# Kernel optimization log

Measured on AMD Instinct MI355X. Metric: run time of the kernel, lower is better.

The kernel has to match this reference:

```python
import jax, jax.numpy as jnp
import numpy as np

B, T, I, H, O = 64, 512, 512, 1024, 512


def _lstm_layer(x_seq, W_ih, W_hh, b_ih, b_hh):
    # x_seq: [B, T, D_in]; PyTorch LSTMCell gate order: i, f, g, o
    bsz = x_seq.shape[0]
    hid = W_hh.shape[1]
    # Precompute input projection for all timesteps as one big GEMM
    x_proj = jnp.einsum('btd,gd->btg', x_seq, W_ih) + b_ih + b_hh  # [B, T, 4H]

    def step(carry, xp_t):
        h, c = carry
        gates = xp_t + h @ W_hh.T  # [B, 4H]
        i_g, f_g, g_g, o_g = jnp.split(gates, 4, axis=-1)
        i_g = jax.nn.sigmoid(i_g)
        f_g = jax.nn.sigmoid(f_g)
        g_g = jnp.tanh(g_g)
        o_g = jax.nn.sigmoid(o_g)
        c_new = f_g * c + i_g * g_g
        h_new = o_g * jnp.tanh(c_new)
        return (h_new, c_new), h_new

    h0 = jnp.zeros((bsz, hid), dtype=x_seq.dtype)
    c0 = jnp.zeros((bsz, hid), dtype=x_seq.dtype)
    (_, _), hs = jax.lax.scan(step, (h0, c0), jnp.swapaxes(x_proj, 0, 1))
    return jnp.swapaxes(hs, 0, 1)  # [B, T, H]


def setup_inputs() -> dict:
    key = jax.random.key(0)
    ks = jax.random.split(key, 12)
    s1 = 1.0 / np.sqrt(H)
    x = jax.random.normal(ks[0], (B, T, I), dtype=jnp.float32)
    W_ih1 = jax.random.uniform(ks[1], (4 * H, I), jnp.float32, -s1, s1)
    W_hh1 = jax.random.uniform(ks[2], (4 * H, H), jnp.float32, -s1, s1)
    b_ih1 = jax.random.uniform(ks[3], (4 * H,), jnp.float32, -s1, s1)
    b_hh1 = jax.random.uniform(ks[4], (4 * H,), jnp.float32, -s1, s1)
    W_ih2 = jax.random.uniform(ks[5], (4 * H, H), jnp.float32, -s1, s1)
    W_hh2 = jax.random.uniform(ks[6], (4 * H, H), jnp.float32, -s1, s1)
    b_ih2 = jax.random.uniform(ks[7], (4 * H,), jnp.float32, -s1, s1)
    b_hh2 = jax.random.uniform(ks[8], (4 * H,), jnp.float32, -s1, s1)
    fc_W = jax.random.uniform(ks[9], (O, H), jnp.float32, -s1, s1)
    fc_b = jax.random.uniform(ks[10], (O,), jnp.float32, -s1, s1)
    return {"x": x, "W_ih1": W_ih1, "W_hh1": W_hh1, "b_ih1": b_ih1, "b_hh1": b_hh1,
            "W_ih2": W_ih2, "W_hh2": W_hh2, "b_ih2": b_ih2, "b_hh2": b_hh2,
            "fc_W": fc_W, "fc_b": fc_b}


def reference(x, W_ih1, W_hh1, b_ih1, b_hh1, W_ih2, W_hh2, b_ih2, b_hh2, fc_W, fc_b):
    h1s = _lstm_layer(x, W_ih1, W_hh1, b_ih1, b_hh1)   # [B, T, H]
    h2s = _lstm_layer(h1s, W_ih2, W_hh2, b_ih2, b_hh2)  # [B, T, H]
    out = jnp.einsum('bth,oh->bto', h2s, fc_W) + fc_b   # [B, T, O]
    return out
```

## Files before the change

kernel.cpp:

```cpp
#include <hip/hip_runtime.h>
#include <hip/hip_bf16.h>
#include <math.h>

#define B_  64
#define T_  512
#define I_  512
#define H_  1024
#define G4_ 4096
#define O_  512
#define TC_ 64
#define NCH (T_ / TC_)
#define WPG 16

typedef short  s16x8 __attribute__((ext_vector_type(8)));
typedef float  fx4   __attribute__((ext_vector_type(4)));
typedef float  fx8   __attribute__((ext_vector_type(8)));
typedef unsigned short u16;
typedef u16    u16x4 __attribute__((ext_vector_type(4)));
typedef unsigned long long u64t;

__device__ __forceinline__ u16 f2bf(float f){
  unsigned u = __float_as_uint(f);
  unsigned r = u + 0x7fffu + ((u >> 16) & 1u);
  return (u16)(r >> 16);
}
__device__ __forceinline__ float bf2f(u16 s){ return __uint_as_float(((unsigned)s) << 16); }
__device__ __forceinline__ float sigm(float x){ return 1.0f / (1.0f + __expf(-x)); }
__device__ __forceinline__ float tanh_(float x){
  float ax = fabsf(x);
  float e  = __expf(2.0f * ax);
  float r  = 1.0f - 2.0f / (e + 1.0f);
  return copysignf(r, x);
}
__device__ __forceinline__ fx4 mfma(s16x8 a, s16x8 b, fx4 c){
  return __builtin_amdgcn_mfma_f32_16x16x32_bf16(a, b, c, 0, 0, 0);
}
__device__ __forceinline__ void keepreg(s16x8& v){ asm volatile("" : "+v"(v)); }

__device__ __forceinline__ void lds_cp16(const u16* g, short* l){
  __builtin_amdgcn_global_load_lds(
      (const __attribute__((address_space(1))) void*)g,
      (__attribute__((address_space(3))) void*)l, 16, 0, 0);
}

__device__ __forceinline__ u64t aload64(const u16* p){
  return __hip_atomic_load((const u64t*)p, __ATOMIC_RELAXED, __HIP_MEMORY_SCOPE_SYSTEM);
}
__device__ __forceinline__ void astore32(u16* p, unsigned v){
  __hip_atomic_store((unsigned*)p, v, __ATOMIC_RELAXED, __HIP_MEMORY_SCOPE_SYSTEM);
}
__device__ __forceinline__ unsigned aload32(const unsigned* p){
  return __hip_atomic_load(p, __ATOMIC_RELAXED, __HIP_MEMORY_SCOPE_SYSTEM);
}
__device__ __forceinline__ unsigned afadd(unsigned* p){
  return __hip_atomic_fetch_add(p, 1u, __ATOMIC_RELAXED, __HIP_MEMORY_SCOPE_SYSTEM);
}

__global__ void cvt_hilo(const float* __restrict__ src, u16* __restrict__ hi,
                         u16* __restrict__ lo, int n4){
  int i      = blockIdx.x * blockDim.x + threadIdx.x;
  int stride = gridDim.x * blockDim.x;
  for (; i < n4; i += stride){
    fx4 v = ((const fx4*)src)[i];
    u16x4 h, l;
    #pragma unroll
    for (int k = 0; k < 4; ++k){
      u16 hh = f2bf(v[k]);
      h[k] = hh;
      l[k] = f2bf(v[k] - bf2f(hh));
    }
    ((u16x4*)hi)[i] = h;
    ((u16x4*)lo)[i] = l;
  }
}

__global__ void vadd(const float* __restrict__ a, const float* __restrict__ b,
                     float* __restrict__ o, int n){
  int i = blockIdx.x * blockDim.x + threadIdx.x;
  if (i < n) o[i] = a[i] + b[i];
}

template<int KD, int AMODE, int OMODE>
__global__ __launch_bounds__(256)
void gemm128(const float* __restrict__ Af,
             const u16* __restrict__ Ah, const u16* __restrict__ Al,
             const u16* __restrict__ Bh, const u16* __restrict__ Bl,
             const float* __restrict__ bias,
             float* __restrict__ out, int N, int c0)
{
  __shared__ short As0[4096], As1[4096];
  __shared__ short Bs0[4096], Bs1[4096];
  __shared__ float xt[(OMODE == 0) ? 64 * 130 : 4];

  const int tid  = threadIdx.x;
  const int w    = tid >> 6;
  const int lane = tid & 63;
  const int l15  = lane & 15;
  const int lhi  = lane >> 4;
  const int mb   = blockIdx.x * 128;
  const int nb   = blockIdx.y * 128;

  const int srow  = lane >> 2;
  const int skc   = lane & 3;
  const int sslot = srow * 32 + skc * 8;

  fx4 acc[4][4] = {};

  for (int kt = 0; kt < KD / 32; ++kt){
    const int kk = kt * 32 + skc * 8;
    __syncthreads();
    #pragma unroll
    for (int bi = 0; bi < 2; ++bi){
      const int bl   = 2 * w + bi;
      const int lrow = bl * 16 + srow;
      const int r    = mb + lrow;
      const int b    = r & 63;
      const int tlr  = r >> 6;
      const size_t bo = (size_t)(nb + bl * 16 + srow) * KD + kk;
      lds_cp16(Bh + bo, &Bs0[bl * 512]);
      lds_cp16(Bl + bo, &Bs1[bl * 512]);
      if (AMODE == 0){
        const float* p = Af + ((size_t)b * T_ + c0 + tlr) * KD + kk;
        fx8 v = *reinterpret_cast<const fx8*>(p);
        s16x8 hv, lv;
        #pragma unroll
        for (int q = 0; q < 8; ++q){
          u16 hh = f2bf(v[q]);
          hv[q] = (short)hh;
          lv[q] = (short)f2bf(v[q] - bf2f(hh));
        }
        *reinterpret_cast<s16x8*>(&As0[bl * 512 + sslot]) = hv;
        *reinterpret_cast<s16x8*>(&As1[bl * 512 + sslot]) = lv;
      } else {
        const size_t ao = ((size_t)b * TC_ + tlr) * KD + kk;
        lds_cp16(Ah + ao, &As0[bl * 512]);
        lds_cp16(Al + ao, &As1[bl * 512]);
      }
    }
    __syncthreads();

    const int fro = l15 * 32 + lhi * 8;
    s16x8 bhf[4], blf[4];
    #pragma unroll
    for (int j = 0; j < 4; ++j){
      const int bb = ((w >> 1) * 4 + j) * 512 + fro;
      bhf[j] = *reinterpret_cast<const s16x8*>(&Bs0[bb]);
      blf[j] = *reinterpret_cast<const s16x8*>(&Bs1[bb]);
    }
    #pragma unroll
    for (int i = 0; i < 4; ++i){
      const int ab = ((w & 1) * 4 + i) * 512 + fro;
      s16x8 ah = *reinterpret_cast<const s16x8*>(&As0[ab]);
      s16x8 al = *reinterpret_cast<const s16x8*>(&As1[ab]);
      #pragma unroll
      for (int j = 0; j < 4; ++j){
        acc[i][j] = mfma(ah, bhf[j], acc[i][j]);
        acc[i][j] = mfma(ah, blf[j], acc[i][j]);
        acc[i][j] = mfma(al, bhf[j], acc[i][j]);
      }
    }
  }

  if (OMODE == 0){
    #pragma unroll
    for (int p = 0; p < 2; ++p){
      __syncthreads();
      if ((w & 1) == p){
        #pragma unroll
        for (int i = 0; i < 4; ++i)
          #pragma unroll
          for (int j = 0; j < 4; ++j){
            const int col = (w >> 1) * 64 + j * 16 + l15;
            const float bv = bias[nb + col];
            #pragma unroll
            for (int r = 0; r < 4; ++r)
              xt[(i * 16 + lhi * 4 + r) * 130 + col] = acc[i][j][r] + bv;
          }
      }
      __syncthreads();
      const int tlv = (mb >> 6) + p;
      const int b   = tid & 63;
      #pragma unroll
      for (int c = 0; c < 32; ++c){
        const int col = (tid >> 6) + c * 4;
        const int n = nb + col;
        const int g = n >> 10;
        const int jj = n & 1023;
        out[((size_t)(tlv * 4 + g) * H_ + jj) * 64 + b] = xt[b * 130 + col];
      }
    }
  } else {
    #pragma unroll
    for (int j = 0; j < 4; ++j){
      const int n = nb + (w >> 1) * 64 + j * 16 + l15;
      const float bv = bias[n];
      #pragma unroll
      for (int i = 0; i < 4; ++i)
        #pragma unroll
        for (int r = 0; r < 4; ++r){
          const int m  = mb + (w & 1) * 64 + i * 16 + lhi * 4 + r;
          const int b  = m & 63;
          const int tlv = m >> 6;
          out[((size_t)b * T_ + c0 + tlv) * (size_t)N + n] = acc[i][j][r] + bv;
        }
    }
  }
}

__device__ __forceinline__ void gbar(unsigned* bar, int gid, unsigned ep, int ngrp){
  if (afadd(&bar[gid * 32]) == WPG - 1u){
    __hip_atomic_store(&bar[gid * 32], 0u, __ATOMIC_RELAXED, __HIP_MEMORY_SCOPE_SYSTEM);
    if (afadd(&bar[512]) == (unsigned)(ngrp - 1)){
      __hip_atomic_store(&bar[512], 0u, __ATOMIC_RELAXED, __HIP_MEMORY_SCOPE_SYSTEM);
      astore32((u16*)&bar[544], ep);
    } else {
      while (aload32(&bar[544]) != ep) __builtin_amdgcn_s_sleep(1);
    }
    astore32((u16*)&bar[1024 + gid * 32], ep);
  } else {
    while (aload32(&bar[1024 + gid * 32]) != ep) __builtin_amdgcn_s_sleep(1);
  }
}

#define RSTR 577
__global__ __launch_bounds__(512) __attribute__((amdgpu_waves_per_eu(2, 2)))
void lstm_pd(int mode, unsigned ep0, int ngrp,
    const u16* __restrict__ W1h, const u16* __restrict__ W1l,
    const float* __restrict__ xp1, float* __restrict__ cst1,
    u16* __restrict__ hx1h, u16* __restrict__ hx1l,
    u16* __restrict__ ha1h, u16* __restrict__ ha1l,
    const u16* __restrict__ W2h, const u16* __restrict__ W2l,
    const float* __restrict__ xp2, float* __restrict__ cst2,
    u16* __restrict__ hx2h, u16* __restrict__ hx2l,
    u16* __restrict__ ha2h, u16* __restrict__ ha2l,
    unsigned* __restrict__ bar)
{
  __shared__ float red[16 * RSTR];

  const int x8 = blockIdx.x & 7;
  const int q  = blockIdx.x >> 3;
  int part, m4, ghi;
  if (mode == 3){ part = q & 1;    m4 = (q >> 1) & 3; ghi = q >> 3; }
  else          { part = mode - 1; m4 = q & 3;        ghi = q >> 2; }
  const int jb  = (x8 + 8 * ghi) * 32;
  const int mb  = m4 * 16;
  const int gid = blockIdx.x >> 4;

  const u16*   Wh  = part ? W2h  : W1h;
  const u16*   Wl  = part ? W2l  : W1l;
  const float* xp  = part ? xp2  : xp1;
  float*       cst = part ? cst2 : cst1;
  u16*         hxh = part ? hx2h : hx1h;
  u16*         hxl = part ? hx2l : hx1l;
  u16*         hah = part ? ha2h : ha1h;
  u16*         hal = part ? ha2l : ha1l;

  const int tid  = threadIdx.x;
  const int lane = tid & 63;
  const int wv   = tid >> 6;
  const int l15  = lane & 15;
  const int lhi  = lane >> 4;
  const int kb0  = wv * 128 + lhi * 8;

  size_t wrowR[4], wrowS[4];
  #pragma unroll
  for (int ct = 0; ct < 4; ++ct){
    const int clR = ct * 16 + l15;
    const int clS = (ct + 4) * 16 + l15;
    wrowR[ct] = (size_t)((clR >> 5) * H_ + jb + (clR & 31));
    wrowS[ct] = (size_t)((clS >> 5) * H_ + jb + (clS & 31));
  }

  s16x8 wrh[4][4], wrl[4][4];
  #pragma unroll
  for (int ct = 0; ct < 4; ++ct)
    #pragma unroll
    for (int s = 0; s < 4; ++s){
      const size_t wo = wrowR[ct] * H_ + kb0 + s * 32;
      wrh[ct][s] = *reinterpret_cast<const s16x8*>(Wh + wo);
      wrl[ct][s] = *reinterpret_cast<const s16x8*>(Wl + wo);
      keepreg(wrh[ct][s]);
      keepreg(wrl[ct][s]);
    }

  const int up = tid & 15;
  const int mm = tid >> 4;
  const int u0 = 2 * up;
  const int j0 = jb + u0;
  const int eb = mb + mm;
  float cva = 0.0f, cvb = 0.0f;
  if (tid < 256){
    cva = cst[(size_t)j0 * B_ + eb];
    cvb = cst[(size_t)(j0 + 1) * B_ + eb];
  }

  for (int tl = 0; tl < TC_; ++tl){
    const int par = tl & 1;
    const u16* rph = hxh + par * (64 * H_);
    const u16* rpl = hxl + par * (64 * H_);
    u16* nph = hxh + (par ^ 1) * (64 * H_);
    u16* npl = hxl + (par ^ 1) * (64 * H_);

    float xq0[4], xq1[4];
    if (tid < 256){
      #pragma unroll
      for (int g = 0; g < 4; ++g){
        const float* xr = xp + ((size_t)(tl * 4 + g) * H_ + j0) * 64 + eb;
        xq0[g] = xr[0];
        xq1[g] = xr[64];
      }
    }

    fx4 acc[8] = {};
    #pragma unroll
    for (int s = 0; s < 4; ++s){
      const int kb = kb0 + s * 32;
      const u16* ph = rph + (size_t)(mb + l15) * H_ + kb;
      const u16* pl = rpl + (size_t)(mb + l15) * H_ + kb;
      union { u64t u[2]; s16x8 v; } ua, ul;
      ua.u[0] = aload64(ph);  ua.u[1] = aload64(ph + 4);
      ul.u[0] = aload64(pl);  ul.u[1] = aload64(pl + 4);
      #pragma unroll
      for (int ct = 0; ct < 4; ++ct){
        acc[ct] = mfma(ua.v, wrh[ct][s], acc[ct]);
        acc[ct] = mfma(ua.v, wrl[ct][s], acc[ct]);
        acc[ct] = mfma(ul.v, wrh[ct][s], acc[ct]);
      }
      #pragma unroll
      for (int ct = 0; ct < 4; ++ct){
        const size_t wo = wrowS[ct] * H_ + kb;
        s16x8 bh = *reinterpret_cast<const s16x8*>(Wh + wo);
        s16x8 bl = *reinterpret_cast<const s16x8*>(Wl + wo);
        acc[4 + ct] = mfma(ua.v, bh, acc[4 + ct]);
        acc[4 + ct] = mfma(ua.v, bl, acc[4 + ct]);
        acc[4 + ct] = mfma(ul.v, bh, acc[4 + ct]);
      }
    }

    #pragma unroll
    for (int ct = 0; ct < 4; ++ct)
      #pragma unroll
      for (int r = 0; r < 4; ++r)
        red[(lhi * 4 + r) * RSTR + (ct * 16 + l15) * 9 + wv] = acc[ct][r];
    __syncthreads();
    float i0s = 0, i1s = 0, f0s = 0, f1s = 0;
    if (tid < 256){
      const float* r0 = red + mm * RSTR + (u0) * 9;
      const float* r1 = red + mm * RSTR + (u0 + 1) * 9;
      const float* r2 = red + mm * RSTR + (32 + u0) * 9;
      const float* r3 = red + mm * RSTR + (32 + u0 + 1) * 9;
      #pragma unroll
      for (int w = 0; w < 8; ++w){
        i0s += r0[w]; i1s += r1[w]; f0s += r2[w]; f1s += r3[w];
      }
    }
    __syncthreads();

    #pragma unroll
    for (int ct = 0; ct < 4; ++ct)
      #pragma unroll
      for (int r = 0; r < 4; ++r)
        red[(lhi * 4 + r) * RSTR + (ct * 16 + l15) * 9 + wv] = acc[4 + ct][r];
    __syncthreads();

    if (tid < 256){
      float g0s = 0, g1s = 0, o0s = 0, o1s = 0;
      const float* r0 = red + mm * RSTR + (u0) * 9;
      const float* r1 = red + mm * RSTR + (u0 + 1) * 9;
      const float* r2 = red + mm * RSTR + (32 + u0) * 9;
      const float* r3 = red + mm * RSTR + (32 + u0 + 1) * 9;
      #pragma unroll
      for (int w = 0; w < 8; ++w){
        g0s += r0[w]; g1s += r1[w]; o0s += r2[w]; o1s += r3[w];
      }
      float iv = sigm (i0s + xq0[0]);
      float fv = sigm (f0s + xq0[1]);
      float gv = tanh_(g0s + xq0[2]);
      float ov = sigm (o0s + xq0[3]);
      float cn = fv * cva + iv * gv;
      float h0 = ov * tanh_(cn);
      cva = cn;
      iv = sigm (i1s + xq1[0]);
      fv = sigm (f1s + xq1[1]);
      gv = tanh_(g1s + xq1[2]);
      ov = sigm (o1s + xq1[3]);
      cn = fv * cvb + iv * gv;
      float h1 = ov * tanh_(cn);
      cvb = cn;

      u16 h0h = f2bf(h0), h0l = f2bf(h0 - bf2f(h0h));
      u16 h1h = f2bf(h1), h1l = f2bf(h1 - bf2f(h1h));
      astore32(nph + (size_t)eb * H_ + j0, (unsigned)h0h | ((unsigned)h1h << 16));
      astore32(npl + (size_t)eb * H_ + j0, (unsigned)h0l | ((unsigned)h1l << 16));
      const size_t ai = ((size_t)eb * TC_ + tl) * H_ + j0;
      *(unsigned*)(hah + ai) = (unsigned)h0h | ((unsigned)h1h << 16);
      *(unsigned*)(hal + ai) = (unsigned)h0l | ((unsigned)h1l << 16);
    }

    __syncthreads();
    if (tid == 0) gbar(bar, gid, ep0 + tl + 1, ngrp);
    __syncthreads();
  }
  if (tid < 256){
    cst[(size_t)j0 * B_ + eb]       = cva;
    cst[(size_t)(j0 + 1) * B_ + eb] = cvb;
  }
}

extern "C" void kernel_launch(void* const* d_in, const int* in_sizes, int n_in,
                              void* d_out, int out_size, void* d_ws, size_t ws_size,
                              hipStream_t stream)
{
  const float* x    = (const float*)d_in[0];
  const float* Wih1 = (const float*)d_in[1];
  const float* Whh1 = (const float*)d_in[2];
  const float* bih1 = (const float*)d_in[3];
  const float* bhh1 = (const float*)d_in[4];
  const float* Wih2 = (const float*)d_in[5];
  const float* Whh2 = (const float*)d_in[6];
  const float* bih2 = (const float*)d_in[7];
  const float* bhh2 = (const float*)d_in[8];
  const float* fcW  = (const float*)d_in[9];
  const float* fcb  = (const float*)d_in[10];
  float* out = (float*)d_out;
  (void)in_sizes; (void)n_in; (void)out_size; (void)ws_size;

  char* base = (char*)d_ws;
  size_t off = 0;
  auto alloc = [&](size_t bytes) -> void* {
    void* p = base + off;
    off = (off + bytes + 255) & ~(size_t)255;
    return p;
  };
  u16* Wih1_hi = (u16*)alloc((size_t)G4_ * I_ * 2);
  u16* Wih1_lo = (u16*)alloc((size_t)G4_ * I_ * 2);
  u16* Whh1_hi = (u16*)alloc((size_t)G4_ * H_ * 2);
  u16* Whh1_lo = (u16*)alloc((size_t)G4_ * H_ * 2);
  u16* Wih2_hi = (u16*)alloc((size_t)G4_ * H_ * 2);
  u16* Wih2_lo = (u16*)alloc((size_t)G4_ * H_ * 2);
  u16* Whh2_hi = (u16*)alloc((size_t)G4_ * H_ * 2);
  u16* Whh2_lo = (u16*)alloc((size_t)G4_ * H_ * 2);
  u16* fcW_hi  = (u16*)alloc((size_t)O_ * H_ * 2);
  u16* fcW_lo  = (u16*)alloc((size_t)O_ * H_ * 2);
  float* bsum1 = (float*)alloc((size_t)G4_ * 4);
  float* bsum2 = (float*)alloc((size_t)G4_ * 4);
  float* cst1  = (float*)alloc((size_t)B_ * H_ * 4);
  float* cst2  = (float*)alloc((size_t)B_ * H_ * 4);
  u16* hx1h = (u16*)alloc((size_t)2 * B_ * H_ * 2);
  u16* hx1l = (u16*)alloc((size_t)2 * B_ * H_ * 2);
  u16* hx2h = (u16*)alloc((size_t)2 * B_ * H_ * 2);
  u16* hx2l = (u16*)alloc((size_t)2 * B_ * H_ * 2);
  u16* h1s_hi = (u16*)alloc((size_t)B_ * TC_ * H_ * 2);
  u16* h1s_lo = (u16*)alloc((size_t)B_ * TC_ * H_ * 2);
  u16* h2s_hi = (u16*)alloc((size_t)B_ * TC_ * H_ * 2);
  u16* h2s_lo = (u16*)alloc((size_t)B_ * TC_ * H_ * 2);
  float* xp1  = (float*)alloc((size_t)TC_ * G4_ * B_ * 4);
  float* xp2  = (float*)alloc((size_t)TC_ * G4_ * B_ * 4);
  unsigned* bar = (unsigned*)alloc(2048 * 4);

  cvt_hilo<<<512, 256, 0, stream>>>(Wih1, Wih1_hi, Wih1_lo, G4_ * I_ / 4);
  cvt_hilo<<<512, 256, 0, stream>>>(Whh1, Whh1_hi, Whh1_lo, G4_ * H_ / 4);
  cvt_hilo<<<512, 256, 0, stream>>>(Wih2, Wih2_hi, Wih2_lo, G4_ * H_ / 4);
  cvt_hilo<<<512, 256, 0, stream>>>(Whh2, Whh2_hi, Whh2_lo, G4_ * H_ / 4);
  cvt_hilo<<<256, 256, 0, stream>>>(fcW,  fcW_hi,  fcW_lo,  O_ * H_ / 4);
  vadd<<<16, 256, 0, stream>>>(bih1, bhh1, bsum1, G4_);
  vadd<<<16, 256, 0, stream>>>(bih2, bhh2, bsum2, G4_);

  hipMemsetAsync(cst1, 0, (size_t)B_ * H_ * 4, stream);
  hipMemsetAsync(cst2, 0, (size_t)B_ * H_ * 4, stream);
  hipMemsetAsync(hx1h, 0, (size_t)2 * B_ * H_ * 2, stream);
  hipMemsetAsync(hx1l, 0, (size_t)2 * B_ * H_ * 2, stream);
  hipMemsetAsync(hx2h, 0, (size_t)2 * B_ * H_ * 2, stream);
  hipMemsetAsync(hx2l, 0, (size_t)2 * B_ * H_ * 2, stream);
  hipMemsetAsync(bar,  0, 2048 * 4, stream);

  const dim3 gX(32, 32);
  const dim3 gF(32, 4);

  gemm128<I_, 0, 0><<<gX, 256, 0, stream>>>(
      x, nullptr, nullptr, Wih1_hi, Wih1_lo, bsum1, xp1, G4_, 0);

  unsigned ep = 0;
  for (int c = 0; c <= NCH; ++c){
    const int mode = ((c < NCH) ? 1 : 0) | ((c >= 1) ? 2 : 0);
    const int nwg  = (mode == 3) ? 256 : 128;
    int ngrp = nwg / WPG;
    {
      void* args[] = { (void*)&mode, (void*)&ep, (void*)&ngrp,
                       (void*)&Whh1_hi, (void*)&Whh1_lo, (void*)&xp1, (void*)&cst1,
                       (void*)&hx1h, (void*)&hx1l, (void*)&h1s_hi, (void*)&h1s_lo,
                       (void*)&Whh2_hi, (void*)&Whh2_lo, (void*)&xp2, (void*)&cst2,
                       (void*)&hx2h, (void*)&hx2l, (void*)&h2s_hi, (void*)&h2s_lo,
                       (void*)&bar };
      hipLaunchCooperativeKernel((const void*)lstm_pd, dim3(nwg), dim3(512),
                                 args, 0, stream);
      ep += TC_;
    }
    if (c < NCH)
      gemm128<H_, 1, 0><<<gX, 256, 0, stream>>>(
          nullptr, h1s_hi, h1s_lo, Wih2_hi, Wih2_lo, bsum2, xp2, G4_, 0);
    if (c + 1 < NCH)
      gemm128<I_, 0, 0><<<gX, 256, 0, stream>>>(
          x, nullptr, nullptr, Wih1_hi, Wih1_lo, bsum1, xp1, G4_, (c + 1) * TC_);
    if (c >= 1)
      gemm128<H_, 1, 1><<<gF, 256, 0, stream>>>(
          nullptr, h2s_hi, h2s_lo, fcW_hi, fcW_lo, fcb, out, O_, (c - 1) * TC_);
  }
}
```

Measured before the change: 10.14 ms.

## Run both LSTM layers in 1024-thread blocks with per-half layer split

The recurrent kernel now always launches 256 workgroups of 1024 threads. Each half of a workgroup handles one LSTM layer, and a mode bit can idle a half. Each block covers 16 hidden units instead of 32, and the weights are streamed from global memory every step instead of being pinned in registers. This is meant to spread the recurrent work across more CUs and cut register pressure. In exchange it reloads weights every timestep, issues narrower 16-bit atomic stores and leaves half-idle blocks in the first and last chunks.

Result: slower. 20.78 ms (+105.0%).

```diff
diff --git a/kernel.cpp b/kernel.cpp
--- a/kernel.cpp
+++ b/kernel.cpp
@@ -35,7 +35,6 @@
 __device__ __forceinline__ fx4 mfma(s16x8 a, s16x8 b, fx4 c){
   return __builtin_amdgcn_mfma_f32_16x16x32_bf16(a, b, c, 0, 0, 0);
 }
-__device__ __forceinline__ void keepreg(s16x8& v){ asm volatile("" : "+v"(v)); }
 
 __device__ __forceinline__ void lds_cp16(const u16* g, short* l){
   __builtin_amdgcn_global_load_lds(
@@ -48,6 +47,9 @@
 }
 __device__ __forceinline__ void astore32(u16* p, unsigned v){
   __hip_atomic_store((unsigned*)p, v, __ATOMIC_RELAXED, __HIP_MEMORY_SCOPE_SYSTEM);
+}
+__device__ __forceinline__ void astore16(u16* p, u16 v){
+  __hip_atomic_store(p, v, __ATOMIC_RELAXED, __HIP_MEMORY_SCOPE_SYSTEM);
 }
 __device__ __forceinline__ unsigned aload32(const unsigned* p){
   return __hip_atomic_load(p, __ATOMIC_RELAXED, __HIP_MEMORY_SCOPE_SYSTEM);
@@ -210,21 +212,21 @@
 __device__ __forceinline__ void gbar(unsigned* bar, int gid, unsigned ep, int ngrp){
   if (afadd(&bar[gid * 32]) == WPG - 1u){
     __hip_atomic_store(&bar[gid * 32], 0u, __ATOMIC_RELAXED, __HIP_MEMORY_SCOPE_SYSTEM);
-    if (afadd(&bar[512]) == (unsigned)(ngrp - 1)){
-      __hip_atomic_store(&bar[512], 0u, __ATOMIC_RELAXED, __HIP_MEMORY_SCOPE_SYSTEM);
-      astore32((u16*)&bar[544], ep);
+    if (afadd(&bar[1024]) == (unsigned)(ngrp - 1)){
+      __hip_atomic_store(&bar[1024], 0u, __ATOMIC_RELAXED, __HIP_MEMORY_SCOPE_SYSTEM);
+      astore32((u16*)&bar[1056], ep);
     } else {
-      while (aload32(&bar[544]) != ep) __builtin_amdgcn_s_sleep(1);
-    }
-    astore32((u16*)&bar[1024 + gid * 32], ep);
+      while (aload32(&bar[1056]) != ep) __builtin_amdgcn_s_sleep(1);
+    }
+    astore32((u16*)&bar[2048 + gid * 32], ep);
   } else {
-    while (aload32(&bar[1024 + gid * 32]) != ep) __builtin_amdgcn_s_sleep(1);
+    while (aload32(&bar[2048 + gid * 32]) != ep) __builtin_amdgcn_s_sleep(1);
   }
 }
 
 #define RSTR 577
-__global__ __launch_bounds__(512) __attribute__((amdgpu_waves_per_eu(2, 2)))
-void lstm_pd(int mode, unsigned ep0, int ngrp,
+__global__ __launch_bounds__(1024)
+void lstm_pd3(int mode, unsigned ep0, int ngrp,
     const u16* __restrict__ W1h, const u16* __restrict__ W1l,
     const float* __restrict__ xp1, float* __restrict__ cst1,
     u16* __restrict__ hx1h, u16* __restrict__ hx1l,
@@ -235,64 +237,46 @@
     u16* __restrict__ ha2h, u16* __restrict__ ha2l,
     unsigned* __restrict__ bar)
 {
-  __shared__ float red[16 * RSTR];
-
-  const int x8 = blockIdx.x & 7;
-  const int q  = blockIdx.x >> 3;
-  int part, m4, ghi;
-  if (mode == 3){ part = q & 1;    m4 = (q >> 1) & 3; ghi = q >> 3; }
-  else          { part = mode - 1; m4 = q & 3;        ghi = q >> 2; }
-  const int jb  = (x8 + 8 * ghi) * 32;
-  const int mb  = m4 * 16;
-  const int gid = blockIdx.x >> 4;
-
-  const u16*   Wh  = part ? W2h  : W1h;
-  const u16*   Wl  = part ? W2l  : W1l;
-  const float* xp  = part ? xp2  : xp1;
-  float*       cst = part ? cst2 : cst1;
-  u16*         hxh = part ? hx2h : hx1h;
-  u16*         hxl = part ? hx2l : hx1l;
-  u16*         hah = part ? ha2h : ha1h;
-  u16*         hal = part ? ha2l : ha1l;
+  __shared__ float red[2][16 * RSTR];
 
   const int tid  = threadIdx.x;
-  const int lane = tid & 63;
-  const int wv   = tid >> 6;
+  const int half = tid >> 9;
+  const int htid = tid & 511;
+  const int act  = (mode >> half) & 1;
+  const int gid  = blockIdx.x >> 4;
+  const int bx   = blockIdx.x;
+  const int m4   = bx & 3;
+  const int ug   = bx >> 2;
+  const int jb   = ug * 16;
+  const int mb   = m4 * 16;
+
+  const u16*   Wh  = half ? W2h  : W1h;
+  const u16*   Wl  = half ? W2l  : W1l;
+  const float* xp  = half ? xp2  : xp1;
+  float*       cst = half ? cst2 : cst1;
+  u16*         hxh = half ? hx2h : hx1h;
+  u16*         hxl = half ? hx2l : hx1l;
+  u16*         hah = half ? ha2h : ha1h;
+  u16*         hal = half ? ha2l : ha1l;
+  float*       rd  = red[half];
+
+  const int lane = htid & 63;
+  const int wv   = htid >> 6;
   const int l15  = lane & 15;
   const int lhi  = lane >> 4;
   const int kb0  = wv * 128 + lhi * 8;
 
-  size_t wrowR[4], wrowS[4];
-  #pragma unroll
-  for (int ct = 0; ct < 4; ++ct){
-    const int clR = ct * 16 + l15;
-    const int clS = (ct + 4) * 16 + l15;
-    wrowR[ct] = (size_t)((clR >> 5) * H_ + jb + (clR & 31));
-    wrowS[ct] = (size_t)((clS >> 5) * H_ + jb + (clS & 31));
-  }
-
-  s16x8 wrh[4][4], wrl[4][4];
+  size_t wrow[4];
   #pragma unroll
   for (int ct = 0; ct < 4; ++ct)
-    #pragma unroll
-    for (int s = 0; s < 4; ++s){
-      const size_t wo = wrowR[ct] * H_ + kb0 + s * 32;
-      wrh[ct][s] = *reinterpret_cast<const s16x8*>(Wh + wo);
-      wrl[ct][s] = *reinterpret_cast<const s16x8*>(Wl + wo);
-      keepreg(wrh[ct][s]);
-      keepreg(wrl[ct][s]);
-    }
-
-  const int up = tid & 15;
-  const int mm = tid >> 4;
-  const int u0 = 2 * up;
-  const int j0 = jb + u0;
+    wrow[ct] = (size_t)(ct * H_ + jb + l15);
+
+  const int uu = htid & 15;
+  const int mm = (htid >> 4) & 15;
+  const int j0 = jb + uu;
   const int eb = mb + mm;
-  float cva = 0.0f, cvb = 0.0f;
-  if (tid < 256){
-    cva = cst[(size_t)j0 * B_ + eb];
-    cvb = cst[(size_t)(j0 + 1) * B_ + eb];
-  }
+  float cva = 0.0f;
+  if (act && htid < 256) cva = cst[(size_t)j0 * B_ + eb];
 
   for (int tl = 0; tl < TC_; ++tl){
     const int par = tl & 1;
@@ -301,110 +285,72 @@
     u16* nph = hxh + (par ^ 1) * (64 * H_);
     u16* npl = hxl + (par ^ 1) * (64 * H_);
 
-    float xq0[4], xq1[4];
-    if (tid < 256){
+    float xq[4];
+    if (act && htid < 256){
+      #pragma unroll
+      for (int g = 0; g < 4; ++g)
+        xq[g] = xp[((size_t)(tl * 4 + g) * H_ + j0) * 64 + eb];
+    }
+
+    if (act){
+      fx4 acc[4] = {};
+      #pragma unroll
+      for (int s = 0; s < 4; ++s){
+        const int kb = kb0 + s * 32;
+        const u16* ph = rph + (size_t)(mb + l15) * H_ + kb;
+        const u16* pl = rpl + (size_t)(mb + l15) * H_ + kb;
+        union { u64t u[2]; s16x8 v; } ua, ul;
+        ua.u[0] = aload64(ph);  ua.u[1] = aload64(ph + 4);
+        ul.u[0] = aload64(pl);  ul.u[1] = aload64(pl + 4);
+        #pragma unroll
+        for (int ct = 0; ct < 4; ++ct){
+          const size_t wo = wrow[ct] * H_ + kb;
+          s16x8 bh = *reinterpret_cast<const s16x8*>(Wh + wo);
+          s16x8 bl = *reinterpret_cast<const s16x8*>(Wl + wo);
+          acc[ct] = mfma(ua.v, bh, acc[ct]);
+          acc[ct] = mfma(ua.v, bl, acc[ct]);
+          acc[ct] = mfma(ul.v, bh, acc[ct]);
+        }
+      }
+      #pragma unroll
+      for (int ct = 0; ct < 4; ++ct)
+        #pragma unroll
+        for (int r = 0; r < 4; ++r)
+          rd[(lhi * 4 + r) * RSTR + (ct * 16 + l15) * 9 + wv] = acc[ct][r];
+    }
+    __syncthreads();
+
+    if (act && htid < 256){
+      float gsum[4];
       #pragma unroll
       for (int g = 0; g < 4; ++g){
-        const float* xr = xp + ((size_t)(tl * 4 + g) * H_ + j0) * 64 + eb;
-        xq0[g] = xr[0];
-        xq1[g] = xr[64];
-      }
-    }
-
-    fx4 acc[8] = {};
-    #pragma unroll
-    for (int s = 0; s < 4; ++s){
-      const int kb = kb0 + s * 32;
-      const u16* ph = rph + (size_t)(mb + l15) * H_ + kb;
-      const u16* pl = rpl + (size_t)(mb + l15) * H_ + kb;
-      union { u64t u[2]; s16x8 v; } ua, ul;
-      ua.u[0] = aload64(ph);  ua.u[1] = aload64(ph + 4);
-      ul.u[0] = aload64(pl);  ul.u[1] = aload64(pl + 4);
-      #pragma unroll
-      for (int ct = 0; ct < 4; ++ct){
-        acc[ct] = mfma(ua.v, wrh[ct][s], acc[ct]);
-        acc[ct] = mfma(ua.v, wrl[ct][s], acc[ct]);
-        acc[ct] = mfma(ul.v, wrh[ct][s], acc[ct]);
-      }
-      #pragma unroll
-      for (int ct = 0; ct < 4; ++ct){
-        const size_t wo = wrowS[ct] * H_ + kb;
-        s16x8 bh = *reinterpret_cast<const s16x8*>(Wh + wo);
-        s16x8 bl = *reinterpret_cast<const s16x8*>(Wl + wo);
-        acc[4 + ct] = mfma(ua.v, bh, acc[4 + ct]);
-        acc[4 + ct] = mfma(ua.v, bl, acc[4 + ct]);
-        acc[4 + ct] = mfma(ul.v, bh, acc[4 + ct]);
-      }
-    }
-
-    #pragma unroll
-    for (int ct = 0; ct < 4; ++ct)
-      #pragma unroll
-      for (int r = 0; r < 4; ++r)
-        red[(lhi * 4 + r) * RSTR + (ct * 16 + l15) * 9 + wv] = acc[ct][r];
-    __syncthreads();
-    float i0s = 0, i1s = 0, f0s = 0, f1s = 0;
-    if (tid < 256){
-      const float* r0 = red + mm * RSTR + (u0) * 9;
-      const float* r1 = red + mm * RSTR + (u0 + 1) * 9;
-      const float* r2 = red + mm * RSTR + (32 + u0) * 9;
-      const float* r3 = red + mm * RSTR + (32 + u0 + 1) * 9;
-      #pragma unroll
-      for (int w = 0; w < 8; ++w){
-        i0s += r0[w]; i1s += r1[w]; f0s += r2[w]; f1s += r3[w];
-      }
-    }
-    __syncthreads();
-
-    #pragma unroll
-    for (int ct = 0; ct < 4; ++ct)
-      #pragma unroll
-      for (int r = 0; r < 4; ++r)
-        red[(lhi * 4 + r) * RSTR + (ct * 16 + l15) * 9 + wv] = acc[4 + ct][r];
-    __syncthreads();
-
-    if (tid < 256){
-      float g0s = 0, g1s = 0, o0s = 0, o1s = 0;
-      const float* r0 = red + mm * RSTR + (u0) * 9;
-      const float* r1 = red + mm * RSTR + (u0 + 1) * 9;
-      const float* r2 = red + mm * RSTR + (32 + u0) * 9;
-      const float* r3 = red + mm * RSTR + (32 + u0 + 1) * 9;
-      #pragma unroll
-      for (int w = 0; w < 8; ++w){
-        g0s += r0[w]; g1s += r1[w]; o0s += r2[w]; o1s += r3[w];
-      }
-      float iv = sigm (i0s + xq0[0]);
-      float fv = sigm (f0s + xq0[1]);
-      float gv = tanh_(g0s + xq0[2]);
-      float ov = sigm (o0s + xq0[3]);
+        const float* rp = rd + mm * RSTR + (g * 16 + uu) * 9;
+        float s = 0.0f;
+        #pragma unroll
+        for (int w = 0; w < 8; ++w) s += rp[w];
+        gsum[g] = s;
+      }
+      float iv = sigm (gsum[0] + xq[0]);
+      float fv = sigm (gsum[1] + xq[1]);
+      float gv = tanh_(gsum[2] + xq[2]);
+      float ov = sigm (gsum[3] + xq[3]);
       float cn = fv * cva + iv * gv;
-      float h0 = ov * tanh_(cn);
+      float hv = ov * tanh_(cn);
       cva = cn;
-      iv = sigm (i1s + xq1[0]);
-      fv = sigm (f1s + xq1[1]);
-      gv = tanh_(g1s + xq1[2]);
-      ov = sigm (o1s + xq1[3]);
-      cn = fv * cvb + iv * gv;
-      float h1 = ov * tanh_(cn);
-      cvb = cn;
-
-      u16 h0h = f2bf(h0), h0l = f2bf(h0 - bf2f(h0h));
-      u16 h1h = f2bf(h1), h1l = f2bf(h1 - bf2f(h1h));
-      astore32(nph + (size_t)eb * H_ + j0, (unsigned)h0h | ((unsigned)h1h << 16));
-      astore32(npl + (size_t)eb * H_ + j0, (unsigned)h0l | ((unsigned)h1l << 16));
+      u16 hh = f2bf(hv);
+      u16 hl = f2bf(hv - bf2f(hh));
+      astore16(nph + (size_t)eb * H_ + j0, hh);
+      astore16(npl + (size_t)eb * H_ + j0, hl);
       const size_t ai = ((size_t)eb * TC_ + tl) * H_ + j0;
-      *(unsigned*)(hah + ai) = (unsigned)h0h | ((unsigned)h1h << 16);
-      *(unsigned*)(hal + ai) = (unsigned)h0l | ((unsigned)h1l << 16);
+      hah[ai] = hh;
+      hal[ai] = hl;
     }
 
     __syncthreads();
     if (tid == 0) gbar(bar, gid, ep0 + tl + 1, ngrp);
     __syncthreads();
   }
-  if (tid < 256){
-    cst[(size_t)j0 * B_ + eb]       = cva;
-    cst[(size_t)(j0 + 1) * B_ + eb] = cvb;
-  }
+  if (act && htid < 256) cst[(size_t)j0 * B_ + eb] = cva;
 }
 
 extern "C" void kernel_launch(void* const* d_in, const int* in_sizes, int n_in,
@@ -456,7 +402,7 @@
   u16* h2s_lo = (u16*)alloc((size_t)B_ * TC_ * H_ * 2);
   float* xp1  = (float*)alloc((size_t)TC_ * G4_ * B_ * 4);
   float* xp2  = (float*)alloc((size_t)TC_ * G4_ * B_ * 4);
-  unsigned* bar = (unsigned*)alloc(2048 * 4);
+  unsigned* bar = (unsigned*)alloc(4096 * 4);
 
   cvt_hilo<<<512, 256, 0, stream>>>(Wih1, Wih1_hi, Wih1_lo, G4_ * I_ / 4);
   cvt_hilo<<<512, 256, 0, stream>>>(Whh1, Whh1_hi, Whh1_lo, G4_ * H_ / 4);
@@ -472,7 +418,7 @@
   hipMemsetAsync(hx1l, 0, (size_t)2 * B_ * H_ * 2, stream);
   hipMemsetAsync(hx2h, 0, (size_t)2 * B_ * H_ * 2, stream);
   hipMemsetAsync(hx2l, 0, (size_t)2 * B_ * H_ * 2, stream);
-  hipMemsetAsync(bar,  0, 2048 * 4, stream);
+  hipMemsetAsync(bar,  0, 4096 * 4, stream);
 
   const dim3 gX(32, 32);
   const dim3 gF(32, 4);
@@ -483,8 +429,7 @@
   unsigned ep = 0;
   for (int c = 0; c <= NCH; ++c){
     const int mode = ((c < NCH) ? 1 : 0) | ((c >= 1) ? 2 : 0);
-    const int nwg  = (mode == 3) ? 256 : 128;
-    int ngrp = nwg / WPG;
+    int ngrp = 16;
     {
       void* args[] = { (void*)&mode, (void*)&ep, (void*)&ngrp,
                        (void*)&Whh1_hi, (void*)&Whh1_lo, (void*)&xp1, (void*)&cst1,
@@ -492,7 +437,7 @@
                        (void*)&Whh2_hi, (void*)&Whh2_lo, (void*)&xp2, (void*)&cst2,
                        (void*)&hx2h, (void*)&hx2l, (void*)&h2s_hi, (void*)&h2s_lo,
                        (void*)&bar };
-      hipLaunchCooperativeKernel((const void*)lstm_pd, dim3(nwg), dim3(512),
+      hipLaunchCooperativeKernel((const void*)lstm_pd3, dim3(256), dim3(1024),
                                  args, 0, stream);
       ep += TC_;
     }
```
